# Performance work log

Hardware: AMD Instinct MI355X
Metric: run time of the kernel (lower is better)

Reference implementation:

```python
import jax, jax.numpy as jnp
import numpy as np

N = 50000      # nodes
E = 1600000    # edges
E_HIDDEN = 256
R_HIDDEN = 128
R = 1000       # number of relations (rel.max()+1)
EPS = 1e-16


def segment_softmax(scores, seg, num_segments):
    # numerically stable softmax over variable-size groups defined by seg
    m = jax.ops.segment_max(scores, seg, num_segments=num_segments)
    ex = jnp.exp(scores - m[seg])
    s = jax.ops.segment_sum(ex, seg, num_segments=num_segments)
    return ex / (s[seg] + EPS)


def setup_inputs() -> dict:
    key = jax.random.key(0)
    ks = jax.random.split(key, 9)
    x_e = jax.random.normal(ks[0], (N, E_HIDDEN), dtype=jnp.float32)
    edge_index = jax.random.randint(ks[1], (2, E), 0, N, dtype=jnp.int64)
    rel = jax.random.randint(ks[2], (E,), 0, R, dtype=jnp.int64)
    # learned params (Linear without bias); stored as [in, out]
    sc_w = 1.0 / np.sqrt(E_HIDDEN)
    sc_a = 1.0 / np.sqrt(R_HIDDEN)
    W_h = jax.random.uniform(ks[3], (E_HIDDEN, R_HIDDEN), jnp.float32, -sc_w, sc_w)
    W_t = jax.random.uniform(ks[4], (E_HIDDEN, R_HIDDEN), jnp.float32, -sc_w, sc_w)
    a_h1 = jax.random.uniform(ks[5], (R_HIDDEN,), jnp.float32, -sc_a, sc_a)
    a_h2 = jax.random.uniform(ks[6], (R_HIDDEN,), jnp.float32, -sc_a, sc_a)
    a_t1 = jax.random.uniform(ks[7], (R_HIDDEN,), jnp.float32, -sc_a, sc_a)
    a_t2 = jax.random.uniform(ks[8], (R_HIDDEN,), jnp.float32, -sc_a, sc_a)
    return {"x_e": x_e, "edge_index": edge_index, "rel": rel,
            "W_h": W_h, "W_t": W_t,
            "a_h1": a_h1, "a_h2": a_h2, "a_t1": a_t1, "a_t2": a_t2}


def reference(x_e, edge_index, rel, W_h, W_t, a_h1, a_h2, a_t1, a_t2):
    h_idx, t_idx = edge_index[0], edge_index[1]
    x_r_h = x_e @ W_h          # [N, r_hidden]
    x_r_t = x_e @ W_t          # [N, r_hidden]
    # per-node scalar scores, gathered per edge
    s_h1 = x_r_h @ a_h1        # [N]
    s_h2 = x_r_t @ a_h2
    s_t1 = x_r_h @ a_t1
    s_t2 = x_r_t @ a_t2
    e1 = s_h1[h_idx] + s_h2[t_idx]   # [E]
    e2 = s_t1[h_idx] + s_t2[t_idx]   # [E]
    alpha1 = segment_softmax(jax.nn.leaky_relu(e1, 0.01), rel, R)
    alpha2 = segment_softmax(jax.nn.leaky_relu(e2, 0.01), rel, R)
    # spmm: out[r] += alpha_e * feat[node_e]
    out_h = jax.ops.segment_sum(alpha1[:, None] * x_r_h[h_idx], rel, num_segments=R)
    out_t = jax.ops.segment_sum(alpha2[:, None] * x_r_t[t_idx], rel, num_segments=R)
    return out_h + out_t       # [R, r_hidden]
```

## Files before the change

### kernel.cpp

```cpp
#include <hip/hip_runtime.h>
#include <hip/hip_fp16.h>
#include <cstdint>
#include <cstddef>

#define E_HID 256
#define R_HID 128
#define NREL  1000
#define EPSF  1e-16f
#define NB    512
#define SPLIT 4

typedef _Float16 f16x8 __attribute__((ext_vector_type(8)));
typedef float f32x4 __attribute__((ext_vector_type(4)));

struct alignas(16) h8 { __half2 a, b, c, d; };
struct alignas(8)  h4s { __half2 a, b; };

__global__ __launch_bounds__(256) void k0_prep(
    const float* __restrict__ Wh, const float* __restrict__ Wt,
    __half* __restrict__ WcT)
{
  const int k = blockIdx.x;
  const int c = threadIdx.x;
  const float v = (c < R_HID) ? Wh[(size_t)k * R_HID + c]
                              : Wt[(size_t)k * R_HID + (c - R_HID)];
  WcT[(size_t)c * E_HID + k] = __float2half(v);
}

__global__ __launch_bounds__(256) void k1_gemm(
    const float* __restrict__ xe, const __half* __restrict__ WcT,
    const float* __restrict__ ah1, const float* __restrict__ ah2,
    const float* __restrict__ at1, const float* __restrict__ at2,
    __half* __restrict__ xhH, __half* __restrict__ xtH,
    float* __restrict__ sh1, float* __restrict__ sh2,
    float* __restrict__ st1, float* __restrict__ st2, int N)
{
  __shared__ __half As[128 * 32];
  __shared__ __half Bs[128 * 32];
  __shared__ float sA[2][128];
  __shared__ float sB[2][128];

  const int tid  = threadIdx.x;
  const int lane = tid & 63;
  const int wid  = tid >> 6;
  const int wr = wid >> 1, wc = wid & 1;
  const int nbm = (N + 127) >> 7;
  const int mb = blockIdx.x % nbm;
  const int cb = blockIdx.x / nbm;
  const int n0 = mb * 128;

  f32x4 acc[4][4];
  #pragma unroll
  for (int m = 0; m < 4; ++m)
    #pragma unroll
    for (int n = 0; n < 4; ++n) acc[m][n] = (f32x4){0.f, 0.f, 0.f, 0.f};

  const int arow = tid >> 1, ah = tid & 1;
  const bool aok = (n0 + arow) < N;
  const float*  xsrc = xe + (size_t)(n0 + arow) * E_HID + ah * 16;
  const __half* bsrc = WcT + ((size_t)(cb * 128 + arow) << 8) + ah * 16;
  __half* Aw = &As[arow * 32 + ah * 16];
  __half* Bw = &Bs[arow * 32 + ah * 16];

  const int fr = lane & 15, fq = lane >> 4;

  for (int kt = 0; kt < 8; ++kt) {
    __syncthreads();
    float4 v0 = make_float4(0,0,0,0), v1 = v0, v2 = v0, v3 = v0;
    if (aok) {
      const float* s = xsrc + kt * 32;
      v0 = *(const float4*)(s);     v1 = *(const float4*)(s + 4);
      v2 = *(const float4*)(s + 8); v3 = *(const float4*)(s + 12);
    }
    h8 p0, p1;
    p0.a = __floats2half2_rn(v0.x, v0.y); p0.b = __floats2half2_rn(v0.z, v0.w);
    p0.c = __floats2half2_rn(v1.x, v1.y); p0.d = __floats2half2_rn(v1.z, v1.w);
    p1.a = __floats2half2_rn(v2.x, v2.y); p1.b = __floats2half2_rn(v2.z, v2.w);
    p1.c = __floats2half2_rn(v3.x, v3.y); p1.d = __floats2half2_rn(v3.z, v3.w);
    *(h8*)(Aw) = p0; *(h8*)(Aw + 8) = p1;
    float4 b0 = *(const float4*)(bsrc + kt * 32);
    float4 b1 = *(const float4*)(bsrc + kt * 32 + 8);
    *(float4*)(Bw) = b0; *(float4*)(Bw + 8) = b1;
    __syncthreads();
    f16x8 aF[4], bF[4];
    #pragma unroll
    for (int m = 0; m < 4; ++m)
      aF[m] = *(const f16x8*)&As[(wr * 64 + m * 16 + fr) * 32 + fq * 8];
    #pragma unroll
    for (int n = 0; n < 4; ++n)
      bF[n] = *(const f16x8*)&Bs[(wc * 64 + n * 16 + fr) * 32 + fq * 8];
    #pragma unroll
    for (int m = 0; m < 4; ++m)
      #pragma unroll
      for (int n = 0; n < 4; ++n)
        acc[m][n] = __builtin_amdgcn_mfma_f32_16x16x32_f16(aF[m], bF[n], acc[m][n], 0, 0, 0);
  }

  __half* dst = (cb == 0) ? xhH : xtH;
  #pragma unroll
  for (int m = 0; m < 4; ++m) {
    const int rl0 = wr * 64 + m * 16 + fq * 4;
    #pragma unroll
    for (int r = 0; r < 4; ++r) {
      const int node = n0 + rl0 + r;
      if (node < N) {
        #pragma unroll
        for (int n = 0; n < 4; ++n)
          dst[(size_t)node * R_HID + wc * 64 + n * 16 + fr] = __float2half(acc[m][n][r]);
      }
    }
  }

  const float* aV1 = (cb == 0) ? ah1 : ah2;
  const float* aV2 = (cb == 0) ? at1 : at2;
  float avA[4], avB[4];
  #pragma unroll
  for (int n = 0; n < 4; ++n) {
    avA[n] = aV1[wc * 64 + n * 16 + fr];
    avB[n] = aV2[wc * 64 + n * 16 + fr];
  }
  #pragma unroll
  for (int m = 0; m < 4; ++m)
    #pragma unroll
    for (int r = 0; r < 4; ++r) {
      float vA = acc[m][0][r]*avA[0] + acc[m][1][r]*avA[1]
               + acc[m][2][r]*avA[2] + acc[m][3][r]*avA[3];
      float vB = acc[m][0][r]*avB[0] + acc[m][1][r]*avB[1]
               + acc[m][2][r]*avB[2] + acc[m][3][r]*avB[3];
      #pragma unroll
      for (int ofs = 1; ofs < 16; ofs <<= 1) {
        vA += __shfl_xor(vA, ofs, 16);
        vB += __shfl_xor(vB, ofs, 16);
      }
      if (fr == 0) {
        const int rl = wr * 64 + m * 16 + fq * 4 + r;
        sA[wc][rl] = vA;
        sB[wc][rl] = vB;
      }
    }
  __syncthreads();
  if (tid < 128 && n0 + tid < N) {
    float* o1 = (cb == 0) ? sh1 : sh2;
    float* o2 = (cb == 0) ? st1 : st2;
    o1[n0 + tid] = sA[0][tid] + sA[1][tid];
    o2[n0 + tid] = sB[0][tid] + sB[1][tid];
  }
}

__global__ __launch_bounds__(256) void k2_hist(
    const int* __restrict__ rel, unsigned* __restrict__ blockCnt, int E)
{
  __shared__ unsigned lcnt[NREL];
  const int tid = threadIdx.x;
  for (int j = tid; j < NREL; j += 256) lcnt[j] = 0u;
  __syncthreads();
  for (int i = blockIdx.x * 256 + tid; i < E; i += NB * 256)
    atomicAdd(&lcnt[rel[i]], 1u);
  __syncthreads();
  for (int j = tid; j < NREL; j += 256)
    blockCnt[(size_t)blockIdx.x * NREL + j] = lcnt[j];
}

__global__ __launch_bounds__(64) void k3a_scan(
    const unsigned* __restrict__ blockCnt, unsigned* __restrict__ pre,
    unsigned* __restrict__ cnt)
{
  const int r = blockIdx.x;
  const int lane = threadIdx.x;
  unsigned running = 0u;
  for (int b0 = 0; b0 < NB; b0 += 64) {
    const int b = b0 + lane;
    unsigned v = blockCnt[(size_t)b * NREL + r];
    unsigned inc = v;
    #pragma unroll
    for (int ofs = 1; ofs < 64; ofs <<= 1) {
      unsigned nv = __shfl_up(inc, ofs, 64);
      if (lane >= ofs) inc += nv;
    }
    pre[(size_t)b * NREL + r] = running + inc - v;
    running += __shfl(inc, 63, 64);
  }
  if (lane == 0) cnt[r] = running;
}

__global__ __launch_bounds__(1024) void k3b_scan(
    const unsigned* __restrict__ cnt, unsigned* __restrict__ offs)
{
  __shared__ unsigned s[1024];
  const int t = threadIdx.x;
  s[t] = (t < NREL) ? cnt[t] : 0u;
  __syncthreads();
  for (int ofs = 1; ofs < 1024; ofs <<= 1) {
    unsigned add = (t >= ofs) ? s[t - ofs] : 0u;
    __syncthreads();
    s[t] += add;
    __syncthreads();
  }
  if (t == 0) offs[0] = 0u;
  if (t < NREL) offs[t + 1] = s[t];
}

__global__ __launch_bounds__(256) void k4_scatter(
    const int* __restrict__ ei, const int* __restrict__ rel,
    const float* __restrict__ sh1, const float* __restrict__ sh2,
    const float* __restrict__ st1, const float* __restrict__ st2,
    const unsigned* __restrict__ offs, const unsigned* __restrict__ pre,
    float4* __restrict__ meta, int E)
{
  __shared__ unsigned lcur[NREL];
  __shared__ unsigned lbase[NREL];
  const int tid = threadIdx.x;
  for (int j = tid; j < NREL; j += 256) {
    lcur[j] = 0u;
    lbase[j] = offs[j] + pre[(size_t)blockIdx.x * NREL + j];
  }
  __syncthreads();
  for (int i = blockIdx.x * 256 + tid; i < E; i += NB * 256) {
    int h = ei[i], t = ei[E + i], r = rel[i];
    float e1 = sh1[h] + sh2[t];
    float e2 = st1[h] + st2[t];
    float l1 = e1 >= 0.f ? e1 : 0.01f * e1;
    float l2 = e2 >= 0.f ? e2 : 0.01f * e2;
    float w1 = expf(l1);
    float w2 = expf(l2);
    unsigned rank = atomicAdd(&lcur[r], 1u);
    unsigned p = lbase[r] + rank;
    meta[p] = make_float4(__int_as_float(h), __int_as_float(t), w1, w2);
  }
}

__global__ __launch_bounds__(256) void k5_reduce(
    const unsigned* __restrict__ offs,
    const float4* __restrict__ meta,
    const __half* __restrict__ xhH, const __half* __restrict__ xtH,
    float* __restrict__ accH, float* __restrict__ accT,
    float* __restrict__ S1, float* __restrict__ S2)
{
  const int r    = blockIdx.x >> 2;
  const int sp   = blockIdx.x & 3;
  const int team = threadIdx.x >> 6;
  const int lane = threadIdx.x & 63;
  const int es   = lane >> 5;
  const int dl   = lane & 31;
  const int d0   = dl * 4;
  const unsigned start = offs[r], end = offs[r + 1];
  const unsigned len = end - start;
  const int ci = sp * 4 + team;
  const unsigned b0 = start + (unsigned)(((unsigned long long)len * ci) >> 4);
  const unsigned b1 = start + (unsigned)(((unsigned long long)len * (ci + 1)) >> 4);

  float a1[4] = {0.f, 0.f, 0.f, 0.f};
  float a2[4] = {0.f, 0.f, 0.f, 0.f};
  float sw1 = 0.f, sw2 = 0.f;

  for (unsigned base = b0; base < b1; base += 8) {
    #pragma unroll
    for (int u = 0; u < 4; ++u) {
      const unsigned idx = base + 2u * u + (unsigned)es;
      if (idx < b1) {
        const float4 md = meta[idx];
        const int h = __float_as_int(md.x);
        const int t = __float_as_int(md.y);
        const float w1 = md.z, w2 = md.w;
        h4s va = *(const h4s*)(xhH + (size_t)h * R_HID + d0);
        h4s vb = *(const h4s*)(xtH + (size_t)t * R_HID + d0);
        float2 fa0 = __half22float2(va.a), fa1 = __half22float2(va.b);
        float2 fb0 = __half22float2(vb.a), fb1 = __half22float2(vb.b);
        a1[0] += w1 * fa0.x; a1[1] += w1 * fa0.y;
        a1[2] += w1 * fa1.x; a1[3] += w1 * fa1.y;
        a2[0] += w2 * fb0.x; a2[1] += w2 * fb0.y;
        a2[2] += w2 * fb1.x; a2[3] += w2 * fb1.y;
        sw1 += w1; sw2 += w2;
      }
    }
  }
  #pragma unroll
  for (int j = 0; j < 4; ++j) {
    a1[j] += __shfl_xor(a1[j], 32);
    a2[j] += __shfl_xor(a2[j], 32);
  }
  sw1 += __shfl_xor(sw1, 32);
  sw2 += __shfl_xor(sw2, 32);
  if (lane < 32) {
    #pragma unroll
    for (int j = 0; j < 4; ++j) {
      atomicAdd(accH + (size_t)r * R_HID + d0 + j, a1[j]);
      atomicAdd(accT + (size_t)r * R_HID + d0 + j, a2[j]);
    }
    if (lane == 0) { atomicAdd(S1 + r, sw1); atomicAdd(S2 + r, sw2); }
  }
}

__global__ __launch_bounds__(256) void k6_final(
    const float* __restrict__ accH, const float* __restrict__ accT,
    const float* __restrict__ S1, const float* __restrict__ S2,
    float* __restrict__ out)
{
  int i = blockIdx.x * 256 + threadIdx.x;
  if (i >= NREL * R_HID) return;
  int r = i >> 7;
  out[i] = accH[i] / (S1[r] + EPSF) + accT[i] / (S2[r] + EPSF);
}

extern "C" void kernel_launch(void* const* d_in, const int* in_sizes, int n_in,
                              void* d_out, int out_size, void* d_ws, size_t ws_size,
                              hipStream_t stream) {
  const float* xe  = (const float*)d_in[0];
  const int*   ei  = (const int*)d_in[1];
  const int*   rel = (const int*)d_in[2];
  const float* Wh  = (const float*)d_in[3];
  const float* Wt  = (const float*)d_in[4];
  const float* ah1 = (const float*)d_in[5];
  const float* ah2 = (const float*)d_in[6];
  const float* at1 = (const float*)d_in[7];
  const float* at2 = (const float*)d_in[8];
  const int N = in_sizes[0] / E_HID;
  const int E = in_sizes[2];

  char* w = (char*)d_ws;
  size_t o = 0;
  auto alloc = [&](size_t bytes) -> void* {
    void* p = w + o;
    o = (o + bytes + 255) & ~(size_t)255;
    return p;
  };
  __half* WcT = (__half*)alloc((size_t)E_HID * E_HID * 2);
  __half* xhH = (__half*)alloc((size_t)N * R_HID * 2);
  __half* xtH = (__half*)alloc((size_t)N * R_HID * 2);
  float* sh1 = (float*)alloc((size_t)N * 4);
  float* sh2 = (float*)alloc((size_t)N * 4);
  float* st1 = (float*)alloc((size_t)N * 4);
  float* st2 = (float*)alloc((size_t)N * 4);
  float4* meta = (float4*)alloc((size_t)E * 16);
  unsigned* blockCnt = (unsigned*)alloc((size_t)NB * NREL * 4);
  unsigned* pre      = (unsigned*)alloc((size_t)NB * NREL * 4);
  unsigned* cnt      = (unsigned*)alloc((size_t)NREL * 4);
  unsigned* offs     = (unsigned*)alloc((size_t)(NREL + 1) * 4);
  const size_t zstart = o;
  float* S1  = (float*)alloc((size_t)NREL * 4);
  float* S2  = (float*)alloc((size_t)NREL * 4);
  float* accH = (float*)alloc((size_t)NREL * R_HID * 4);
  float* accT = (float*)alloc((size_t)NREL * R_HID * 4);
  const size_t zbytes = o - zstart;

  hipMemsetAsync(w + zstart, 0, zbytes, stream);

  const int nbm = (N + 127) >> 7;
  k0_prep<<<E_HID, 256, 0, stream>>>(Wh, Wt, WcT);
  k1_gemm<<<nbm * 2, 256, 0, stream>>>(xe, WcT, ah1, ah2, at1, at2,
                                       xhH, xtH, sh1, sh2, st1, st2, N);
  k2_hist<<<NB, 256, 0, stream>>>(rel, blockCnt, E);
  k3a_scan<<<NREL, 64, 0, stream>>>(blockCnt, pre, cnt);
  k3b_scan<<<1, 1024, 0, stream>>>(cnt, offs);
  k4_scatter<<<NB, 256, 0, stream>>>(ei, rel, sh1, sh2, st1, st2,
                                     offs, pre, meta, E);
  k5_reduce<<<NREL * SPLIT, 256, 0, stream>>>(offs, meta, xhH, xtH,
                                              accH, accT, S1, S2);
  k6_final<<<(NREL * R_HID + 255) / 256, 256, 0, stream>>>(accH, accT, S1, S2,
                                                           (float*)d_out);
}
```

Baseline: 264.2 us.

## Bucket edges by node chunk and relation for cache-local gathers

Edges are now sorted into separate head and tail lists, bucketed by (node chunk of 4096, relation), using global-atomic histograms and a single-block scan. The reduce kernel walks chunks so the gathered feature rows for one chunk stay cache-resident. It accumulates per-relation-tile sums in shared memory and writes partials, which a final kernel sums, replacing global float atomics. The costs are global atomics in the histogram and scatter, a serial 13k-bin scan in one block, non-deterministic ordering within each bucket, and an extra partial-buffer pass.

```diff
diff --git a/kernel.cpp b/kernel.cpp
--- a/kernel.cpp
+++ b/kernel.cpp
@@ -7,14 +7,20 @@
 #define R_HID 128
 #define NREL  1000
 #define EPSF  1e-16f
-#define NB    512
-#define SPLIT 4
+
+#define CH_BITS 12
+#define CHUNK   (1 << CH_BITS)
+#define NCH     13
+#define NBIN    (NCH * NREL)
+#define RT      32
+#define NRT     32
+#define REP     16
+#define G5      (2 * NRT * REP)
 
 typedef _Float16 f16x8 __attribute__((ext_vector_type(8)));
 typedef float f32x4 __attribute__((ext_vector_type(4)));
 
 struct alignas(16) h8 { __half2 a, b, c, d; };
-struct alignas(8)  h4s { __half2 a, b; };
 
 __global__ __launch_bounds__(256) void k0_prep(
     const float* __restrict__ Wh, const float* __restrict__ Wt,
@@ -148,158 +154,173 @@
 }
 
 __global__ __launch_bounds__(256) void k2_hist(
-    const int* __restrict__ rel, unsigned* __restrict__ blockCnt, int E)
-{
-  __shared__ unsigned lcnt[NREL];
-  const int tid = threadIdx.x;
-  for (int j = tid; j < NREL; j += 256) lcnt[j] = 0u;
-  __syncthreads();
-  for (int i = blockIdx.x * 256 + tid; i < E; i += NB * 256)
-    atomicAdd(&lcnt[rel[i]], 1u);
-  __syncthreads();
-  for (int j = tid; j < NREL; j += 256)
-    blockCnt[(size_t)blockIdx.x * NREL + j] = lcnt[j];
-}
-
-__global__ __launch_bounds__(64) void k3a_scan(
-    const unsigned* __restrict__ blockCnt, unsigned* __restrict__ pre,
-    unsigned* __restrict__ cnt)
-{
-  const int r = blockIdx.x;
-  const int lane = threadIdx.x;
-  unsigned running = 0u;
-  for (int b0 = 0; b0 < NB; b0 += 64) {
-    const int b = b0 + lane;
-    unsigned v = blockCnt[(size_t)b * NREL + r];
-    unsigned inc = v;
-    #pragma unroll
-    for (int ofs = 1; ofs < 64; ofs <<= 1) {
-      unsigned nv = __shfl_up(inc, ofs, 64);
-      if (lane >= ofs) inc += nv;
-    }
-    pre[(size_t)b * NREL + r] = running + inc - v;
-    running += __shfl(inc, 63, 64);
-  }
-  if (lane == 0) cnt[r] = running;
-}
-
-__global__ __launch_bounds__(1024) void k3b_scan(
-    const unsigned* __restrict__ cnt, unsigned* __restrict__ offs)
+    const int* __restrict__ ei, const int* __restrict__ rel,
+    unsigned* __restrict__ cntH, unsigned* __restrict__ cntT, int E)
+{
+  for (int i = blockIdx.x * 256 + threadIdx.x; i < E; i += gridDim.x * 256) {
+    const int r = rel[i];
+    const int h = ei[i], t = ei[E + i];
+    atomicAdd(cntH + (h >> CH_BITS) * NREL + r, 1u);
+    atomicAdd(cntT + (t >> CH_BITS) * NREL + r, 1u);
+  }
+}
+
+__global__ __launch_bounds__(1024) void k3_scan(
+    const unsigned* __restrict__ cntH, const unsigned* __restrict__ cntT,
+    unsigned* __restrict__ offsH, unsigned* __restrict__ offsT,
+    unsigned* __restrict__ curH, unsigned* __restrict__ curT)
 {
   __shared__ unsigned s[1024];
   const int t = threadIdx.x;
-  s[t] = (t < NREL) ? cnt[t] : 0u;
-  __syncthreads();
-  for (int ofs = 1; ofs < 1024; ofs <<= 1) {
-    unsigned add = (t >= ofs) ? s[t - ofs] : 0u;
+  for (int list = 0; list < 2; ++list) {
+    const unsigned* cnt = list ? cntT : cntH;
+    unsigned* offs = list ? offsT : offsH;
+    unsigned* cur  = list ? curT  : curH;
+    unsigned carry = 0u;
+    for (int base = 0; base < NBIN; base += 1024) {
+      const int idx = base + t;
+      const unsigned v = (idx < NBIN) ? cnt[idx] : 0u;
+      s[t] = v;
+      __syncthreads();
+      for (int ofs = 1; ofs < 1024; ofs <<= 1) {
+        unsigned add = (t >= ofs) ? s[t - ofs] : 0u;
+        __syncthreads();
+        s[t] += add;
+        __syncthreads();
+      }
+      if (idx < NBIN) {
+        const unsigned excl = carry + s[t] - v;
+        offs[idx] = excl;
+        cur[idx]  = excl;
+      }
+      carry += s[1023];
+      __syncthreads();
+    }
+    if (t == 0) offs[NBIN] = carry;
     __syncthreads();
-    s[t] += add;
-    __syncthreads();
-  }
-  if (t == 0) offs[0] = 0u;
-  if (t < NREL) offs[t + 1] = s[t];
+  }
 }
 
 __global__ __launch_bounds__(256) void k4_scatter(
     const int* __restrict__ ei, const int* __restrict__ rel,
     const float* __restrict__ sh1, const float* __restrict__ sh2,
     const float* __restrict__ st1, const float* __restrict__ st2,
-    const unsigned* __restrict__ offs, const unsigned* __restrict__ pre,
-    float4* __restrict__ meta, int E)
-{
-  __shared__ unsigned lcur[NREL];
-  __shared__ unsigned lbase[NREL];
-  const int tid = threadIdx.x;
-  for (int j = tid; j < NREL; j += 256) {
-    lcur[j] = 0u;
-    lbase[j] = offs[j] + pre[(size_t)blockIdx.x * NREL + j];
-  }
+    unsigned* __restrict__ curH, unsigned* __restrict__ curT,
+    uint2* __restrict__ metaH, uint2* __restrict__ metaT, int E)
+{
+  for (int i = blockIdx.x * 256 + threadIdx.x; i < E; i += gridDim.x * 256) {
+    const int h = ei[i], t = ei[E + i], r = rel[i];
+    const float e1 = sh1[h] + sh2[t];
+    const float e2 = st1[h] + st2[t];
+    const float l1 = e1 >= 0.f ? e1 : 0.01f * e1;
+    const float l2 = e2 >= 0.f ? e2 : 0.01f * e2;
+    const float w1 = expf(l1);
+    const float w2 = expf(l2);
+    const unsigned pH = atomicAdd(curH + (h >> CH_BITS) * NREL + r, 1u);
+    metaH[pH] = make_uint2((unsigned)((h & (CHUNK - 1)) | ((r & (RT - 1)) << CH_BITS)),
+                           __float_as_uint(w1));
+    const unsigned pT = atomicAdd(curT + (t >> CH_BITS) * NREL + r, 1u);
+    metaT[pT] = make_uint2((unsigned)((t & (CHUNK - 1)) | ((r & (RT - 1)) << CH_BITS)),
+                           __float_as_uint(w2));
+  }
+}
+
+#define FLUSH() do { \
+    if (curRl >= 0) { \
+      atomicAdd(&acc[curRl * 129 + 2 * lane],     a0); \
+      atomicAdd(&acc[curRl * 129 + 2 * lane + 1], a1); \
+      if (lane == 0) atomicAdd(&accS[curRl], sw); \
+    } a0 = 0.f; a1 = 0.f; sw = 0.f; } while (0)
+
+#define EDGE(MV, VV) do { \
+    const int rl = (int)(MV.x >> CH_BITS); \
+    const float w = __uint_as_float(MV.y); \
+    if (rl != curRl) { FLUSH(); curRl = rl; } \
+    const float2 f = __half22float2(VV); \
+    a0 += w * f.x; a1 += w * f.y; sw += w; } while (0)
+
+__global__ __launch_bounds__(256) void k5_reduce(
+    const unsigned* __restrict__ offsH, const unsigned* __restrict__ offsT,
+    const uint2* __restrict__ metaH, const uint2* __restrict__ metaT,
+    const __half* __restrict__ xhH, const __half* __restrict__ xtH,
+    float* __restrict__ part, float* __restrict__ partS)
+{
+  __shared__ float acc[RT * 129];
+  __shared__ float accS[RT];
+  const int tid  = threadIdx.x;
+  const int lane = tid & 63;
+  const int wv   = tid >> 6;
+  const int bid  = blockIdx.x;
+  const int table = bid >> 9;
+  const int rtile = (bid >> 4) & 31;
+  const int rep   = bid & 15;
+
+  for (int i = tid; i < RT * 129; i += 256) acc[i] = 0.f;
+  if (tid < RT) accS[tid] = 0.f;
   __syncthreads();
-  for (int i = blockIdx.x * 256 + tid; i < E; i += NB * 256) {
-    int h = ei[i], t = ei[E + i], r = rel[i];
-    float e1 = sh1[h] + sh2[t];
-    float e2 = st1[h] + st2[t];
-    float l1 = e1 >= 0.f ? e1 : 0.01f * e1;
-    float l2 = e2 >= 0.f ? e2 : 0.01f * e2;
-    float w1 = expf(l1);
-    float w2 = expf(l2);
-    unsigned rank = atomicAdd(&lcur[r], 1u);
-    unsigned p = lbase[r] + rank;
-    meta[p] = make_float4(__int_as_float(h), __int_as_float(t), w1, w2);
-  }
-}
-
-__global__ __launch_bounds__(256) void k5_reduce(
-    const unsigned* __restrict__ offs,
-    const float4* __restrict__ meta,
-    const __half* __restrict__ xhH, const __half* __restrict__ xtH,
-    float* __restrict__ accH, float* __restrict__ accT,
-    float* __restrict__ S1, float* __restrict__ S2)
-{
-  const int r    = blockIdx.x >> 2;
-  const int sp   = blockIdx.x & 3;
-  const int team = threadIdx.x >> 6;
-  const int lane = threadIdx.x & 63;
-  const int es   = lane >> 5;
-  const int dl   = lane & 31;
-  const int d0   = dl * 4;
-  const unsigned start = offs[r], end = offs[r + 1];
-  const unsigned len = end - start;
-  const int ci = sp * 4 + team;
-  const unsigned b0 = start + (unsigned)(((unsigned long long)len * ci) >> 4);
-  const unsigned b1 = start + (unsigned)(((unsigned long long)len * (ci + 1)) >> 4);
-
-  float a1[4] = {0.f, 0.f, 0.f, 0.f};
-  float a2[4] = {0.f, 0.f, 0.f, 0.f};
-  float sw1 = 0.f, sw2 = 0.f;
-
-  for (unsigned base = b0; base < b1; base += 8) {
-    #pragma unroll
-    for (int u = 0; u < 4; ++u) {
-      const unsigned idx = base + 2u * u + (unsigned)es;
-      if (idx < b1) {
-        const float4 md = meta[idx];
-        const int h = __float_as_int(md.x);
-        const int t = __float_as_int(md.y);
-        const float w1 = md.z, w2 = md.w;
-        h4s va = *(const h4s*)(xhH + (size_t)h * R_HID + d0);
-        h4s vb = *(const h4s*)(xtH + (size_t)t * R_HID + d0);
-        float2 fa0 = __half22float2(va.a), fa1 = __half22float2(va.b);
-        float2 fb0 = __half22float2(vb.a), fb1 = __half22float2(vb.b);
-        a1[0] += w1 * fa0.x; a1[1] += w1 * fa0.y;
-        a1[2] += w1 * fa1.x; a1[3] += w1 * fa1.y;
-        a2[0] += w2 * fb0.x; a2[1] += w2 * fb0.y;
-        a2[2] += w2 * fb1.x; a2[3] += w2 * fb1.y;
-        sw1 += w1; sw2 += w2;
-      }
-    }
-  }
-  #pragma unroll
-  for (int j = 0; j < 4; ++j) {
-    a1[j] += __shfl_xor(a1[j], 32);
-    a2[j] += __shfl_xor(a2[j], 32);
-  }
-  sw1 += __shfl_xor(sw1, 32);
-  sw2 += __shfl_xor(sw2, 32);
-  if (lane < 32) {
-    #pragma unroll
-    for (int j = 0; j < 4; ++j) {
-      atomicAdd(accH + (size_t)r * R_HID + d0 + j, a1[j]);
-      atomicAdd(accT + (size_t)r * R_HID + d0 + j, a2[j]);
-    }
-    if (lane == 0) { atomicAdd(S1 + r, sw1); atomicAdd(S2 + r, sw2); }
-  }
-}
-
-__global__ __launch_bounds__(256) void k6_final(
-    const float* __restrict__ accH, const float* __restrict__ accT,
-    const float* __restrict__ S1, const float* __restrict__ S2,
+
+  const unsigned* offs = table ? offsT : offsH;
+  const uint2*    meta = table ? metaT : metaH;
+  const __half*   xsrc = table ? xtH   : xhH;
+  const int r0   = rtile * RT;
+  const int rend = (r0 + RT < NREL) ? r0 + RT : NREL;
+
+  float a0 = 0.f, a1 = 0.f, sw = 0.f;
+  int curRl = -1;
+
+  for (int c = 0; c < NCH; ++c) {
+    const unsigned s0 = offs[c * NREL + r0];
+    const unsigned s1 = offs[c * NREL + rend];
+    const unsigned len = s1 - s0;
+    const unsigned b0 = s0 + ((len * (unsigned)rep) >> 4);
+    const unsigned b1 = s0 + ((len * (unsigned)(rep + 1)) >> 4);
+    const unsigned wl = b1 - b0;
+    unsigned p        = b0 + ((wl * (unsigned)wv) >> 2);
+    const unsigned pe = b0 + ((wl * (unsigned)(wv + 1)) >> 2);
+    const __half* xb = xsrc + (((size_t)c << CH_BITS) * R_HID) + 2 * lane;
+
+    for (; p + 4 <= pe; p += 4) {
+      const uint2 m0 = meta[p],     m1 = meta[p + 1];
+      const uint2 m2 = meta[p + 2], m3 = meta[p + 3];
+      const __half2 v0 = *(const __half2*)(xb + (size_t)(m0.x & (CHUNK - 1)) * R_HID);
+      const __half2 v1 = *(const __half2*)(xb + (size_t)(m1.x & (CHUNK - 1)) * R_HID);
+      const __half2 v2 = *(const __half2*)(xb + (size_t)(m2.x & (CHUNK - 1)) * R_HID);
+      const __half2 v3 = *(const __half2*)(xb + (size_t)(m3.x & (CHUNK - 1)) * R_HID);
+      EDGE(m0, v0); EDGE(m1, v1); EDGE(m2, v2); EDGE(m3, v3);
+    }
+    for (; p < pe; ++p) {
+      const uint2 m = meta[p];
+      const __half2 v = *(const __half2*)(xb + (size_t)(m.x & (CHUNK - 1)) * R_HID);
+      EDGE(m, v);
+    }
+  }
+  FLUSH();
+  __syncthreads();
+
+  float* pd = part + (size_t)bid * (RT * R_HID);
+  for (int i = tid; i < RT * R_HID; i += 256)
+    pd[i] = acc[(i >> 7) * 129 + (i & 127)];
+  if (tid < RT) partS[bid * RT + tid] = accS[tid];
+}
+
+__global__ __launch_bounds__(128) void k6_final(
+    const float* __restrict__ part, const float* __restrict__ partS,
     float* __restrict__ out)
 {
-  int i = blockIdx.x * 256 + threadIdx.x;
-  if (i >= NREL * R_HID) return;
-  int r = i >> 7;
-  out[i] = accH[i] / (S1[r] + EPSF) + accT[i] / (S2[r] + EPSF);
+  const int r = blockIdx.x;
+  const int d = threadIdx.x;
+  const int rtile = r >> 5, rl = r & (RT - 1);
+  float s1 = 0.f, s2 = 0.f, oh = 0.f, ot = 0.f;
+  #pragma unroll
+  for (int rep = 0; rep < REP; ++rep) {
+    const int pid0 = (rtile) * REP + rep;
+    const int pid1 = (NRT + rtile) * REP + rep;
+    oh += part[(size_t)pid0 * (RT * R_HID) + rl * R_HID + d];
+    ot += part[(size_t)pid1 * (RT * R_HID) + rl * R_HID + d];
+    s1 += partS[pid0 * RT + rl];
+    s2 += partS[pid1 * RT + rl];
+  }
+  out[r * R_HID + d] = oh / (s1 + EPSF) + ot / (s2 + EPSF);
 }
 
 extern "C" void kernel_launch(void* const* d_in, const int* in_sizes, int n_in,
@@ -331,16 +352,17 @@
   float* sh2 = (float*)alloc((size_t)N * 4);
   float* st1 = (float*)alloc((size_t)N * 4);
   float* st2 = (float*)alloc((size_t)N * 4);
-  float4* meta = (float4*)alloc((size_t)E * 16);
-  unsigned* blockCnt = (unsigned*)alloc((size_t)NB * NREL * 4);
-  unsigned* pre      = (unsigned*)alloc((size_t)NB * NREL * 4);
-  unsigned* cnt      = (unsigned*)alloc((size_t)NREL * 4);
-  unsigned* offs     = (unsigned*)alloc((size_t)(NREL + 1) * 4);
+  uint2* metaH = (uint2*)alloc((size_t)E * 8);
+  uint2* metaT = (uint2*)alloc((size_t)E * 8);
+  unsigned* offsH = (unsigned*)alloc((size_t)(NBIN + 1) * 4);
+  unsigned* offsT = (unsigned*)alloc((size_t)(NBIN + 1) * 4);
+  float* part  = (float*)alloc((size_t)G5 * RT * R_HID * 4);
+  float* partS = (float*)alloc((size_t)G5 * RT * 4);
   const size_t zstart = o;
-  float* S1  = (float*)alloc((size_t)NREL * 4);
-  float* S2  = (float*)alloc((size_t)NREL * 4);
-  float* accH = (float*)alloc((size_t)NREL * R_HID * 4);
-  float* accT = (float*)alloc((size_t)NREL * R_HID * 4);
+  unsigned* cntH = (unsigned*)alloc((size_t)NBIN * 4);
+  unsigned* cntT = (unsigned*)alloc((size_t)NBIN * 4);
+  unsigned* curH = (unsigned*)alloc((size_t)NBIN * 4);
+  unsigned* curT = (unsigned*)alloc((size_t)NBIN * 4);
   const size_t zbytes = o - zstart;
 
   hipMemsetAsync(w + zstart, 0, zbytes, stream);
@@ -349,13 +371,11 @@
   k0_prep<<<E_HID, 256, 0, stream>>>(Wh, Wt, WcT);
   k1_gemm<<<nbm * 2, 256, 0, stream>>>(xe, WcT, ah1, ah2, at1, at2,
                                        xhH, xtH, sh1, sh2, st1, st2, N);
-  k2_hist<<<NB, 256, 0, stream>>>(rel, blockCnt, E);
-  k3a_scan<<<NREL, 64, 0, stream>>>(blockCnt, pre, cnt);
-  k3b_scan<<<1, 1024, 0, stream>>>(cnt, offs);
-  k4_scatter<<<NB, 256, 0, stream>>>(ei, rel, sh1, sh2, st1, st2,
-                                     offs, pre, meta, E);
-  k5_reduce<<<NREL * SPLIT, 256, 0, stream>>>(offs, meta, xhH, xtH,
-                                              accH, accT, S1, S2);
-  k6_final<<<(NREL * R_HID + 255) / 256, 256, 0, stream>>>(accH, accT, S1, S2,
-                                                           (float*)d_out);
-}
+  k2_hist<<<1024, 256, 0, stream>>>(ei, rel, cntH, cntT, E);
+  k3_scan<<<1, 1024, 0, stream>>>(cntH, cntT, offsH, offsT, curH, curT);
+  k4_scatter<<<1024, 256, 0, stream>>>(ei, rel, sh1, sh2, st1, st2,
+                                       curH, curT, metaH, metaT, E);
+  k5_reduce<<<G5, 256, 0, stream>>>(offsH, offsT, metaH, metaT, xhH, xtH,
+                                    part, partS);
+  k6_final<<<NREL, 128, 0, stream>>>(part, partS, (float*)d_out);
+}
```

Measured after the change: 585.6 us. +121.7%, slower.
